# Kernel tuning notes

Hardware: AMD Instinct MI355X
Metric: run time of the kernel (lower is better)

Reference implementation:

```python
import jax, jax.numpy as jnp
import numpy as np

H = 16          # n_heads
D_MODEL = 1024
DK = D_MODEL // H  # 64
N = 2048        # total tokens (module flattens batch*seq)
NEG = -1000000000.0


def setup_inputs() -> dict:
    key = jax.random.key(0)
    ks = jax.random.split(key, 12)
    s = 1.0 / np.sqrt(D_MODEL)
    inp = {
        "query": jax.random.normal(ks[0], (N, D_MODEL), jnp.float32),
        "key": jax.random.normal(ks[1], (N, D_MODEL), jnp.float32),
        "value": jax.random.normal(ks[2], (N, D_MODEL), jnp.float32),
        "mask": jax.random.randint(ks[3], (1, N), 0, 2, jnp.int32),
        "Wq": jax.random.normal(ks[4], (D_MODEL, D_MODEL), jnp.float32) * s,
        "bq": jax.random.normal(ks[5], (D_MODEL,), jnp.float32) * 0.01,
        "Wk": jax.random.normal(ks[6], (D_MODEL, D_MODEL), jnp.float32) * s,
        "bk": jax.random.normal(ks[7], (D_MODEL,), jnp.float32) * 0.01,
        "Wv": jax.random.normal(ks[8], (D_MODEL, D_MODEL), jnp.float32) * s,
        "bv": jax.random.normal(ks[9], (D_MODEL,), jnp.float32) * 0.01,
        "Wo": jax.random.normal(ks[10], (D_MODEL, D_MODEL), jnp.float32) * s,
        "bo": jax.random.normal(ks[11], (D_MODEL,), jnp.float32) * 0.01,
    }
    return inp


def reference(query, key, value, mask, Wq, bq, Wk, bk, Wv, bv, Wo, bo):
    # Linear projections (torch Linear: x @ W.T + b), then split heads: (N, d_model) -> (h, N, d_k)
    def split_heads(x):
        return x.reshape(-1, H, DK).transpose(1, 0, 2)

    q = split_heads(query @ Wq.T + bq)
    k = split_heads(key @ Wk.T + bk)
    v = split_heads(value @ Wv.T + bv)

    # scaled dot-product attention: scores (h, N, N)
    scores = jnp.einsum("hnd,hmd->hnm", q, k) / jnp.sqrt(jnp.asarray(DK, q.dtype))
    # mask: (1, N) --unsqueeze(1)--> (1, 1, N), broadcast over (h, N, N)
    scores = jnp.where(mask[None, :, :] == 0, jnp.asarray(NEG, scores.dtype), scores)
    p_attn = jax.nn.softmax(scores, axis=-1)  # dropout identity (eval mode)

    x = jnp.einsum("hnm,hmd->hnd", p_attn, v)  # (h, N, d_k)
    x = x.transpose(1, 0, 2).reshape(-1, H * DK)  # (N, d_model)
    out = x @ Wo.T + bo
    return (out, p_attn)
```

## Files before the change

kernel.cpp:

```cpp
#include <hip/hip_runtime.h>


#define NTOK 2048
#define DMODEL 1024
#define NHEAD 16
#define DKH 64

typedef __attribute__((ext_vector_type(8))) short bf16x8;
typedef __attribute__((ext_vector_type(4))) float f32x4;
typedef __attribute__((ext_vector_type(2))) float f32x2;

__device__ __forceinline__ unsigned short f2bf(float x) {
  unsigned int u = __builtin_bit_cast(unsigned int, x);
  u += 0x7fffu + ((u >> 16) & 1u);
  return (unsigned short)(u >> 16);
}

__device__ __forceinline__ void gl16(const void* g, void* l) {
  __builtin_amdgcn_global_load_lds((const __attribute__((address_space(1))) void*)g,
                                   (__attribute__((address_space(3))) void*)l, 16, 0, 0);
}

template<int ROWS>
__device__ __forceinline__ void stage_async(const unsigned short* src, int ld,
                                            char* lds, int w, int lane) {
  constexpr int RPW = ROWS / 4;
#pragma unroll
  for (int i = 0; i < RPW / 8; ++i) {
    const int row = w * RPW + i * 8 + (lane >> 3);
    const unsigned short* g = src + (size_t)row * ld + (((lane & 7) ^ (row & 7)) * 8);
    gl16(g, lds + (size_t)(w * RPW + i * 8) * 128);
  }
}

__device__ __forceinline__ void stage_v(const unsigned short* src, char* lds, int w, int lane) {
#pragma unroll
  for (int i = 0; i < 4; ++i) {
    const int row = w * 16 + i * 4 + (lane >> 4);
    const int ck = lane & 15;
    const unsigned short* g = src + (size_t)row * NTOK + ((ck ^ (row & 7)) * 8);
    gl16(g, lds + (size_t)(w * 16 + i * 4) * 256);
  }
}

__device__ __forceinline__ bf16x8 ldsfrag(const char* lds, int r, int kb) {
  return *(const bf16x8*)(lds + r * 128 + (kb ^ ((r & 7) << 4)));
}
__device__ __forceinline__ bf16x8 ldsfrag256(const char* lds, int r, int kb) {
  return *(const bf16x8*)(lds + r * 256 + (kb ^ ((r & 7) << 4)));
}

struct CvtP {
  const float* src[7];
  unsigned short* dst[7];
  int n8[8];
  const int* mask;
  float* mbias;
};
__global__ __launch_bounds__(256) void cvt_all(CvtP P) {
  const int a = blockIdx.z;
  const int i = blockIdx.x * 256 + threadIdx.x;
  if (i >= P.n8[a]) return;
  if (a == 7) {
#pragma unroll
    for (int r = 0; r < 8; ++r) {
      int j = i * 8 + r;
      P.mbias[j] = P.mask[j] ? 0.0f : -1e30f;
    }
    return;
  }
  const float4* s = (const float4*)P.src[a];
  float4 v0 = s[i * 2], v1 = s[i * 2 + 1];
  ushort4 h0, h1;
  h0.x = f2bf(v0.x); h0.y = f2bf(v0.y); h0.z = f2bf(v0.z); h0.w = f2bf(v0.w);
  h1.x = f2bf(v1.x); h1.y = f2bf(v1.y); h1.z = f2bf(v1.z); h1.w = f2bf(v1.w);
  ((ushort4*)P.dst[a])[i * 2] = h0;
  ((ushort4*)P.dst[a])[i * 2 + 1] = h1;
}

struct GemmP2 {
  const unsigned short* A[3];
  const unsigned short* B[3];
  const float* bias[3];
  unsigned short* Cb16;
  float* Cf32;
  unsigned short* VTd;
  long long sC;
  int lda, ldb, ldc, Nn, K;
};

template<int BM, bool OUTF32, bool VTRANS>
__global__ __launch_bounds__(256) void gemm_glds(GemmP2 P) {
  constexpr int BN = 128, WN = 64, FN = 4;
  constexpr int WM = BM / 2, FM = WM / 16;
  __shared__ char ldsA[BM * 128];
  __shared__ char ldsB[BN * 128];
  const int tid = threadIdx.x;
  const int lane = tid & 63, w = tid >> 6;
  const int l15 = lane & 15, lhi = lane >> 4;
  const int z = blockIdx.z;
  const int zi = (gridDim.z == 3) ? z : 0;
  const int ntn = P.Nn / BN;
  const int m0 = ((int)blockIdx.x / ntn) * BM;
  const int n0 = ((int)blockIdx.x % ntn) * BN;
  const unsigned short* Ab = P.A[zi] + (size_t)m0 * P.lda;
  const unsigned short* Bb = P.B[zi] + (size_t)n0 * P.ldb;
  const int wm = w >> 1, wn = w & 1;

  f32x4 acc[FM][FN] = {};
  for (int k0 = 0; k0 < P.K; k0 += 64) {
    stage_async<BM>(Ab + k0, P.lda, ldsA, w, lane);
    stage_async<BN>(Bb + k0, P.ldb, ldsB, w, lane);
    __syncthreads();
#pragma unroll
    for (int kk = 0; kk < 2; ++kk) {
      const int kb = kk * 64 + lhi * 16;
      bf16x8 a[FM], b[FN];
#pragma unroll
      for (int i = 0; i < FM; ++i) a[i] = ldsfrag(ldsA, wm * WM + i * 16 + l15, kb);
#pragma unroll
      for (int j = 0; j < FN; ++j) b[j] = ldsfrag(ldsB, wn * WN + j * 16 + l15, kb);
#pragma unroll
      for (int i = 0; i < FM; ++i)
#pragma unroll
        for (int j = 0; j < FN; ++j)
          acc[i][j] = __builtin_amdgcn_mfma_f32_16x16x32_bf16(a[i], b[j], acc[i][j], 0, 0, 0);
    }
    __syncthreads();
  }

  const int rbase = m0 + wm * WM + lhi * 4;
  const int cbase = n0 + wn * WN + l15;
  if (VTRANS && z == 2) {
#pragma unroll
    for (int j = 0; j < FN; ++j) {
      const int col = cbase + j * 16;
      const float badd = P.bias[zi][col];
#pragma unroll
      for (int i = 0; i < FM; ++i) {
        ushort4 t;
        t.x = f2bf(acc[i][j][0] + badd); t.y = f2bf(acc[i][j][1] + badd);
        t.z = f2bf(acc[i][j][2] + badd); t.w = f2bf(acc[i][j][3] + badd);
        *(ushort4*)(P.VTd + (size_t)col * NTOK + rbase + i * 16) = t;
      }
    }
    return;
  }
#pragma unroll
  for (int j = 0; j < FN; ++j) {
    const int col = cbase + j * 16;
    const float badd = P.bias[zi] ? P.bias[zi][col] : 0.0f;
#pragma unroll
    for (int i = 0; i < FM; ++i) {
#pragma unroll
      for (int rg = 0; rg < 4; ++rg) {
        const int row = rbase + i * 16 + rg;
        const float v = acc[i][j][rg] + badd;
        if constexpr (OUTF32)
          P.Cf32[(size_t)row * P.ldc + col] = v;
        else
          P.Cb16[(size_t)z * P.sC + (size_t)row * P.ldc + col] = f2bf(v);
      }
    }
  }
}

__global__ __launch_bounds__(256) void attn4(const unsigned short* __restrict__ QP,
                                             const unsigned short* __restrict__ KP,
                                             const unsigned short* __restrict__ VT,
                                             const float* __restrict__ mbias,
                                             float* __restrict__ p,
                                             unsigned short* __restrict__ XB) {
  __shared__ char ldsK[2][128 * 128];
  __shared__ char ldsV[2][64 * 256];
  __shared__ char ldsP[64 * 256];
  const int tid = threadIdx.x;
  const int lane = tid & 63, w = tid >> 6;
  const int l15 = lane & 15, lhi = lane >> 4;
  const int id = blockIdx.x;
  const int h = 2 * (id & 7) + ((id >> 3) & 1);
  const int q0 = (id >> 4) * 64;
  const int mrow = w * 16 + l15;
  constexpr float CEXP = 0.1803368801111204f;

  stage_async<64>(QP + (size_t)q0 * DMODEL + h * DKH, DMODEL, (char*)ldsP, w, lane);
  __syncthreads();
  bf16x8 qf0 = ldsfrag((char*)ldsP, mrow, lhi * 16);
  bf16x8 qf1 = ldsfrag((char*)ldsP, mrow, 64 + lhi * 16);

  const unsigned short* Kh = KP + h * DKH;
  const unsigned short* Vh = VT + (size_t)h * DKH * NTOK;

  float rsum = 0.0f;
  __syncthreads();
  stage_async<128>(Kh, DMODEL, ldsK[0], w, lane);
  __syncthreads();
  int b = 0;
  for (int it = 0; it < 16; ++it) {
    if (it < 15)
      stage_async<128>(Kh + (size_t)(it + 1) * 128 * DMODEL, DMODEL, ldsK[b ^ 1], w, lane);
    f32x4 sacc[8] = {};
#pragma unroll
    for (int kk = 0; kk < 2; ++kk)
#pragma unroll
      for (int js = 0; js < 8; ++js) {
        bf16x8 kf = ldsfrag(ldsK[b], js * 16 + l15, kk * 64 + lhi * 16);
        sacc[js] = __builtin_amdgcn_mfma_f32_16x16x32_bf16(kf, kk ? qf1 : qf0, sacc[js], 0, 0, 0);
      }
    const float* mb = mbias + it * 128;
#pragma unroll
    for (int js = 0; js < 8; ++js) {
      float4 m4 = *(const float4*)(mb + js * 16 + lhi * 4);
      rsum += exp2f(sacc[js][0] * CEXP + m4.x);
      rsum += exp2f(sacc[js][1] * CEXP + m4.y);
      rsum += exp2f(sacc[js][2] * CEXP + m4.z);
      rsum += exp2f(sacc[js][3] * CEXP + m4.w);
    }
    __syncthreads();
    b ^= 1;
  }
  rsum += __shfl_xor(rsum, 16, 64);
  rsum += __shfl_xor(rsum, 32, 64);
  const float lr = -log2f(rsum);

  f32x4 xacc[4] = {};
  stage_async<128>(Kh, DMODEL, ldsK[0], w, lane);
  stage_v(Vh, ldsV[0], w, lane);
  __syncthreads();
  b = 0;
  for (int it = 0; it < 16; ++it) {
    const int j0 = it * 128;
    if (it < 15) {
      stage_async<128>(Kh + (size_t)(j0 + 128) * DMODEL, DMODEL, ldsK[b ^ 1], w, lane);
      stage_v(Vh + j0 + 128, ldsV[b ^ 1], w, lane);
    }
    f32x4 sacc[8] = {};
#pragma unroll
    for (int kk = 0; kk < 2; ++kk)
#pragma unroll
      for (int js = 0; js < 8; ++js) {
        bf16x8 kf = ldsfrag(ldsK[b], js * 16 + l15, kk * 64 + lhi * 16);
        sacc[js] = __builtin_amdgcn_mfma_f32_16x16x32_bf16(kf, kk ? qf1 : qf0, sacc[js], 0, 0, 0);
      }
    const float* mb = mbias + j0;
#pragma unroll
    for (int js = 0; js < 8; ++js) {
      float4 m4 = *(const float4*)(mb + js * 16 + lhi * 4);
      ushort4 pb;
      pb.x = f2bf(exp2f(sacc[js][0] * CEXP + (m4.x + lr)));
      pb.y = f2bf(exp2f(sacc[js][1] * CEXP + (m4.y + lr)));
      pb.z = f2bf(exp2f(sacc[js][2] * CEXP + (m4.z + lr)));
      pb.w = f2bf(exp2f(sacc[js][3] * CEXP + (m4.w + lr)));
      *(ushort4*)(ldsP + mrow * 256 + ((js * 32 + lhi * 8) ^ ((mrow & 7) << 4))) = pb;
    }
#pragma unroll
    for (int jk = 0; jk < 4; ++jk) {
      bf16x8 pf = ldsfrag256(ldsP, mrow, jk * 64 + lhi * 16);
#pragma unroll
      for (int dd = 0; dd < 4; ++dd) {
        bf16x8 vf = ldsfrag256(ldsV[b], dd * 16 + l15, jk * 64 + lhi * 16);
        xacc[dd] = __builtin_amdgcn_mfma_f32_16x16x32_bf16(vf, pf, xacc[dd], 0, 0, 0);
      }
    }
#pragma unroll
    for (int r = 0; r < 16; ++r) {
      const int row = w * 16 + r;
      const unsigned int u =
          *(const unsigned int*)(ldsP + row * 256 + ((lane * 4) ^ ((row & 7) << 4)));
      f32x2 f;
      f[0] = __builtin_bit_cast(float, u << 16);
      f[1] = __builtin_bit_cast(float, u & 0xffff0000u);
      __builtin_nontemporal_store(
          f, (f32x2*)(p + ((size_t)h * NTOK + q0 + row) * NTOK + j0 + lane * 2));
    }
    __syncthreads();
    b ^= 1;
  }

  unsigned short* xrow = XB + (size_t)(q0 + mrow) * DMODEL + h * DKH;
#pragma unroll
  for (int dd = 0; dd < 4; ++dd) {
    ushort4 xb;
    xb.x = f2bf(xacc[dd][0]); xb.y = f2bf(xacc[dd][1]);
    xb.z = f2bf(xacc[dd][2]); xb.w = f2bf(xacc[dd][3]);
    *(ushort4*)(xrow + dd * 16 + lhi * 4) = xb;
  }
}

extern "C" void kernel_launch(void* const* d_in, const int* in_sizes, int n_in,
                              void* d_out, int out_size, void* d_ws, size_t ws_size,
                              hipStream_t stream) {
  (void)in_sizes; (void)n_in; (void)out_size; (void)ws_size;
  const float* query = (const float*)d_in[0];
  const float* key_  = (const float*)d_in[1];
  const float* value = (const float*)d_in[2];
  const int*   mask  = (const int*)d_in[3];
  const float* Wq = (const float*)d_in[4];
  const float* bq = (const float*)d_in[5];
  const float* Wk = (const float*)d_in[6];
  const float* bk = (const float*)d_in[7];
  const float* Wv = (const float*)d_in[8];
  const float* bv = (const float*)d_in[9];
  const float* Wo = (const float*)d_in[10];
  const float* bo = (const float*)d_in[11];

  float* out = (float*)d_out;
  float* p = out + (size_t)NTOK * DMODEL;

  char* ws = (char*)d_ws;
  unsigned short* QP  = (unsigned short*)(ws);
  unsigned short* KP  = (unsigned short*)(ws + (4u << 20));
  unsigned short* VT  = (unsigned short*)(ws + (8u << 20));
  unsigned short* XB  = (unsigned short*)(ws + (12u << 20));
  unsigned short* qB  = (unsigned short*)(ws + (16u << 20));
  unsigned short* kB  = (unsigned short*)(ws + (20u << 20));
  unsigned short* vB  = (unsigned short*)(ws + (24u << 20));
  unsigned short* WqB = (unsigned short*)(ws + (28u << 20));
  unsigned short* WkB = (unsigned short*)(ws + (30u << 20));
  unsigned short* WvB = (unsigned short*)(ws + (32u << 20));
  unsigned short* WoB = (unsigned short*)(ws + (34u << 20));
  float* mbias = (float*)(ws + (36u << 20));

  {
    CvtP C = {};
    C.src[0] = query; C.dst[0] = qB;  C.n8[0] = NTOK * DMODEL / 8;
    C.src[1] = key_;  C.dst[1] = kB;  C.n8[1] = NTOK * DMODEL / 8;
    C.src[2] = value; C.dst[2] = vB;  C.n8[2] = NTOK * DMODEL / 8;
    C.src[3] = Wq;    C.dst[3] = WqB; C.n8[3] = DMODEL * DMODEL / 8;
    C.src[4] = Wk;    C.dst[4] = WkB; C.n8[4] = DMODEL * DMODEL / 8;
    C.src[5] = Wv;    C.dst[5] = WvB; C.n8[5] = DMODEL * DMODEL / 8;
    C.src[6] = Wo;    C.dst[6] = WoB; C.n8[6] = DMODEL * DMODEL / 8;
    C.n8[7] = NTOK / 8;
    C.mask = mask; C.mbias = mbias;
    cvt_all<<<dim3(1024, 1, 8), 256, 0, stream>>>(C);
  }
  {
    GemmP2 P = {};
    P.A[0] = qB; P.A[1] = kB; P.A[2] = vB;
    P.B[0] = WqB; P.B[1] = WkB; P.B[2] = WvB;
    P.bias[0] = bq; P.bias[1] = bk; P.bias[2] = bv;
    P.Cb16 = QP; P.VTd = VT; P.sC = (long long)NTOK * DMODEL;
    P.lda = DMODEL; P.ldb = DMODEL; P.ldc = DMODEL; P.Nn = DMODEL; P.K = DMODEL;
    gemm_glds<128, false, true>
        <<<dim3((NTOK / 128) * (DMODEL / 128), 1, 3), 256, 0, stream>>>(P);
  }
  attn4<<<dim3(512), 256, 0, stream>>>(QP, KP, VT, mbias, p, XB);
  {
    GemmP2 P = {};
    P.A[0] = XB; P.B[0] = WoB; P.bias[0] = bo;
    P.Cf32 = out; P.sC = 0;
    P.lda = DMODEL; P.ldb = DMODEL; P.ldc = DMODEL; P.Nn = DMODEL; P.K = DMODEL;
    gemm_glds<64, true, false>
        <<<dim3((NTOK / 64) * (DMODEL / 128), 1, 1), 256, 0, stream>>>(P);
  }
}
```

Measured before the change: 156.6 us.

## Replace attention syncthreads with vmcnt waits, one barrier per iteration, wider P stores

The attention kernel now synchronizes once per loop iteration, with an explicit s_waitcnt vmcnt plus s_barrier at the top, instead of full __syncthreads before and after each tile. This lets the prefetch of the next K/V tile stay in flight across the compute. In the second pass, vmcnt(8) waits only for the tile loads and leaves the eight probability stores outstanding. The probability write-back now uses 16-byte f32x4 nontemporal stores over 8 iterations instead of 8-byte stores over 16, and it is issued before the PV MFMAs. These changes rely on the exact vmcnt accounting and on sched_barrier placement, which makes the code fragile if the compiler or instruction counts change.

Result: faster. 147.1 us (-6.0%).

```diff
diff --git a/kernel.cpp b/kernel.cpp
--- a/kernel.cpp
+++ b/kernel.cpp
@@ -8,7 +8,17 @@
 
 typedef __attribute__((ext_vector_type(8))) short bf16x8;
 typedef __attribute__((ext_vector_type(4))) float f32x4;
-typedef __attribute__((ext_vector_type(2))) float f32x2;
+
+#define WAITVMC(n)                                          \
+  do {                                                      \
+    asm volatile("s_waitcnt vmcnt(" n ")" ::: "memory");    \
+    __builtin_amdgcn_sched_barrier(0);                      \
+  } while (0)
+#define BARRIER()                                           \
+  do {                                                      \
+    __builtin_amdgcn_s_barrier();                           \
+    __builtin_amdgcn_sched_barrier(0);                      \
+  } while (0)
 
 __device__ __forceinline__ unsigned short f2bf(float x) {
   unsigned int u = __builtin_bit_cast(unsigned int, x);
@@ -165,7 +175,7 @@
   }
 }
 
-__global__ __launch_bounds__(256) void attn4(const unsigned short* __restrict__ QP,
+__global__ __launch_bounds__(256) void attn5(const unsigned short* __restrict__ QP,
                                              const unsigned short* __restrict__ KP,
                                              const unsigned short* __restrict__ VT,
                                              const float* __restrict__ mbias,
@@ -183,22 +193,23 @@
   const int mrow = w * 16 + l15;
   constexpr float CEXP = 0.1803368801111204f;
 
-  stage_async<64>(QP + (size_t)q0 * DMODEL + h * DKH, DMODEL, (char*)ldsP, w, lane);
+  stage_async<64>(QP + (size_t)q0 * DMODEL + h * DKH, DMODEL, ldsP, w, lane);
   __syncthreads();
-  bf16x8 qf0 = ldsfrag((char*)ldsP, mrow, lhi * 16);
-  bf16x8 qf1 = ldsfrag((char*)ldsP, mrow, 64 + lhi * 16);
+  bf16x8 qf0 = ldsfrag(ldsP, mrow, lhi * 16);
+  bf16x8 qf1 = ldsfrag(ldsP, mrow, 64 + lhi * 16);
 
   const unsigned short* Kh = KP + h * DKH;
   const unsigned short* Vh = VT + (size_t)h * DKH * NTOK;
 
   float rsum = 0.0f;
-  __syncthreads();
   stage_async<128>(Kh, DMODEL, ldsK[0], w, lane);
-  __syncthreads();
   int b = 0;
   for (int it = 0; it < 16; ++it) {
+    WAITVMC("0");
+    BARRIER();
     if (it < 15)
       stage_async<128>(Kh + (size_t)(it + 1) * 128 * DMODEL, DMODEL, ldsK[b ^ 1], w, lane);
+    __builtin_amdgcn_sched_barrier(0);
     f32x4 sacc[8] = {};
 #pragma unroll
     for (int kk = 0; kk < 2; ++kk)
@@ -216,7 +227,6 @@
       rsum += exp2f(sacc[js][2] * CEXP + m4.z);
       rsum += exp2f(sacc[js][3] * CEXP + m4.w);
     }
-    __syncthreads();
     b ^= 1;
   }
   rsum += __shfl_xor(rsum, 16, 64);
@@ -226,14 +236,16 @@
   f32x4 xacc[4] = {};
   stage_async<128>(Kh, DMODEL, ldsK[0], w, lane);
   stage_v(Vh, ldsV[0], w, lane);
-  __syncthreads();
   b = 0;
   for (int it = 0; it < 16; ++it) {
     const int j0 = it * 128;
+    if (it == 0) { WAITVMC("0"); } else { WAITVMC("8"); }
+    BARRIER();
     if (it < 15) {
       stage_async<128>(Kh + (size_t)(j0 + 128) * DMODEL, DMODEL, ldsK[b ^ 1], w, lane);
       stage_v(Vh + j0 + 128, ldsV[b ^ 1], w, lane);
     }
+    __builtin_amdgcn_sched_barrier(0);
     f32x4 sacc[8] = {};
 #pragma unroll
     for (int kk = 0; kk < 2; ++kk)
@@ -254,6 +266,19 @@
       *(ushort4*)(ldsP + mrow * 256 + ((js * 32 + lhi * 8) ^ ((mrow & 7) << 4))) = pb;
     }
 #pragma unroll
+    for (int r = 0; r < 8; ++r) {
+      const int row = w * 16 + r * 2 + (lane >> 5);
+      const uint2 u =
+          *(const uint2*)(ldsP + row * 256 + (((lane & 31) * 8) ^ ((row & 7) << 4)));
+      f32x4 f;
+      f[0] = __builtin_bit_cast(float, u.x << 16);
+      f[1] = __builtin_bit_cast(float, u.x & 0xffff0000u);
+      f[2] = __builtin_bit_cast(float, u.y << 16);
+      f[3] = __builtin_bit_cast(float, u.y & 0xffff0000u);
+      __builtin_nontemporal_store(
+          f, (f32x4*)(p + ((size_t)h * NTOK + q0 + row) * NTOK + j0 + (lane & 31) * 4));
+    }
+#pragma unroll
     for (int jk = 0; jk < 4; ++jk) {
       bf16x8 pf = ldsfrag256(ldsP, mrow, jk * 64 + lhi * 16);
 #pragma unroll
@@ -262,18 +287,6 @@
         xacc[dd] = __builtin_amdgcn_mfma_f32_16x16x32_bf16(vf, pf, xacc[dd], 0, 0, 0);
       }
     }
-#pragma unroll
-    for (int r = 0; r < 16; ++r) {
-      const int row = w * 16 + r;
-      const unsigned int u =
-          *(const unsigned int*)(ldsP + row * 256 + ((lane * 4) ^ ((row & 7) << 4)));
-      f32x2 f;
-      f[0] = __builtin_bit_cast(float, u << 16);
-      f[1] = __builtin_bit_cast(float, u & 0xffff0000u);
-      __builtin_nontemporal_store(
-          f, (f32x2*)(p + ((size_t)h * NTOK + q0 + row) * NTOK + j0 + lane * 2));
-    }
-    __syncthreads();
     b ^= 1;
   }
 
@@ -344,7 +357,7 @@
     gemm_glds<128, false, true>
         <<<dim3((NTOK / 128) * (DMODEL / 128), 1, 3), 256, 0, stream>>>(P);
   }
-  attn4<<<dim3(512), 256, 0, stream>>>(QP, KP, VT, mbias, p, XB);
+  attn5<<<dim3(512), 256, 0, stream>>>(QP, KP, VT, mbias, p, XB);
   {
     GemmP2 P = {};
     P.A[0] = XB; P.B[0] = WoB; P.bias[0] = bo;
```
